# Optimization experiments

Measured on AMD Instinct MI355X. Metric: run time of the kernel, lower is better.

## Reference

```python
import jax, jax.numpy as jnp
import numpy as np

P = 16           # patch size
D = 768          # embed / feature dim (= 3*P*P)
T = 8            # number of task vectors
H_META = 192     # MetaNet hidden (= D // 4)


def patchify(x):
    # x: [B, 3, H, W] -> [B, N, 3*P*P]
    B, C, H, W = x.shape
    x = x.reshape(B, C, H // P, P, W // P, P)
    x = x.transpose(0, 2, 4, 1, 3, 5)
    return x.reshape(B, (H // P) * (W // P), C * P * P)


def encode(W1, b1, W2, b2, x):
    # base functional encoder f(params, x): shared weights over the batch
    patches = patchify(x)                       # [B, N, D]
    h = jax.nn.relu(patches @ W1 + b1)          # [B, N, D]
    pooled = h.mean(axis=1)                     # [B, D]
    return pooled @ W2 + b2                     # [B, D]


def setup_inputs() -> dict:
    key = jax.random.key(0)
    ks = jax.random.split(key, 14)
    B = 64
    s = 0.02
    return {
        "x":   jax.random.normal(ks[0], (B, 3, 224, 224), jnp.float32),
        # base model params
        "W1":  jax.random.normal(ks[1], (D, D), jnp.float32) * s,
        "b1":  jax.random.normal(ks[2], (D,), jnp.float32) * s,
        "W2":  jax.random.normal(ks[3], (D, D), jnp.float32) * s,
        "b2":  jax.random.normal(ks[4], (D,), jnp.float32) * s,
        # task-vector deltas (stacked over T tasks)
        "dW1": jax.random.normal(ks[5], (T, D, D), jnp.float32) * s,
        "db1": jax.random.normal(ks[6], (T, D), jnp.float32) * s,
        "dW2": jax.random.normal(ks[7], (T, D, D), jnp.float32) * s,
        "db2": jax.random.normal(ks[8], (T, D), jnp.float32) * s,
        # MetaNet (Linear-ReLU-Linear); zero-init in the original, random here
        "mw1": jax.random.normal(ks[9], (D, H_META), jnp.float32) * s,
        "mb1": jax.random.normal(ks[10], (H_META,), jnp.float32) * s,
        "mw2": jax.random.normal(ks[11], (H_META, T), jnp.float32) * s,
        "mb2": jax.random.normal(ks[12], (T,), jnp.float32) * s,
    }


def reference(x, W1, b1, W2, b2, dW1, db1, dW2, db2, mw1, mb1, mw2, mb2):
    # 1) base features with frozen base model (torch.no_grad)
    base = jax.lax.stop_gradient(encode(W1, b1, W2, b2, x))       # [B, D]
    # 2) per-sample mixing coefficients via MetaNet
    coefs = jax.nn.relu(base @ mw1 + mb1) @ mw2 + mb2             # [B, T]
    # 3) per-sample mixed parameters: p + sum_t c[b,t] * dp[t]
    nW1 = W1 + jnp.einsum("bt,tij->bij", coefs, dW1)              # [B, D, D]
    nb1 = b1 + coefs @ db1                                        # [B, D]
    nW2 = W2 + jnp.einsum("bt,tij->bij", coefs, dW2)              # [B, D, D]
    nb2 = b2 + coefs @ db2                                        # [B, D]
    # 4) batched per-sample forward with the mixed weights
    patches = patchify(x)                                         # [B, N, D]
    h = jax.nn.relu(jnp.einsum("bnd,bde->bne", patches, nW1) + nb1[:, None, :])
    pooled = h.mean(axis=1)                                       # [B, D]
    out = jnp.einsum("bd,bde->be", pooled, nW2) + nb2             # [B, D]
    return out
```

## Files before the change

kernel.cpp:

```cpp
#include <hip/hip_runtime.h>
#include <hip/hip_bf16.h>


typedef __bf16 bf16x8 __attribute__((ext_vector_type(8)));
typedef float f32x4 __attribute__((ext_vector_type(4)));
typedef __hip_bfloat16 bf16;

struct alignas(16) BF8 { bf16 h[8]; };

constexpr int BATCH = 64;
constexpr int NP    = 196;
constexpr int NPAD  = 256;
constexpr int DIM   = 768;
constexpr int NT    = 8;
constexpr size_t MSZ = (size_t)DIM * DIM;

__device__ __forceinline__ void async_cp16(const void* g, void* l) {
  __builtin_amdgcn_global_load_lds(
      (const __attribute__((address_space(1))) uint32_t*)g,
      (__attribute__((address_space(3))) uint32_t*)l, 16, 0, 0);
}

#define WAITVM(N) asm volatile("s_waitcnt vmcnt(" #N ")" ::: "memory")

constexpr int PREP_PATCH_BLOCKS = (BATCH * NPAD * (DIM / 4)) / 256;
constexpr int PREP_TRANS_BLOCKS = 24 * 24 * 18;

__global__ void k_prep(const float* __restrict__ x, bf16* __restrict__ A,
                       const float* __restrict__ W1, const float* __restrict__ dW1,
                       const float* __restrict__ W2, const float* __restrict__ dW2,
                       bf16* __restrict__ WT) {
  __shared__ float tile[32][33];
  int blk = blockIdx.x;
  int tid = threadIdx.x;
  if (blk < PREP_PATCH_BLOCKS) {
    int idx  = blk * 256 + tid;
    int col4 = idx % (DIM / 4);
    int row  = idx / (DIM / 4);
    int d = col4 * 4;
    int b = row >> 8;
    int n = row & 255;
    bf16 tmp[4];
    if (n < NP) {
      int hp = n / 14, wp = n % 14;
      int c  = d >> 8;
      int rr = d & 255;
      int i = rr >> 4, j = rr & 15;
      const float* src = x + ((((size_t)b * 3 + c) * 224 + hp * 16 + i) * 224 + wp * 16 + j);
      float4 f = *(const float4*)src;
      tmp[0] = __float2bfloat16(f.x);
      tmp[1] = __float2bfloat16(f.y);
      tmp[2] = __float2bfloat16(f.z);
      tmp[3] = __float2bfloat16(f.w);
    } else {
      tmp[0] = tmp[1] = tmp[2] = tmp[3] = __float2bfloat16(0.0f);
    }
    *(ushort4*)(A + (size_t)row * DIM + d) = *(ushort4*)tmp;
  } else {
    int tb  = blk - PREP_PATCH_BLOCKS;
    int mat = tb / 576;
    int rem = tb % 576;
    int n0 = (rem % 24) * 32;
    int k0 = (rem / 24) * 32;
    const float* src;
    if      (mat == 0) src = W1;
    else if (mat <= 8) src = dW1 + (size_t)(mat - 1) * MSZ;
    else if (mat == 9) src = W2;
    else               src = dW2 + (size_t)(mat - 10) * MSZ;
    int tx = tid & 31, ty = tid >> 5;
#pragma unroll
    for (int r = ty; r < 32; r += 8)
      tile[r][tx] = src[(size_t)(k0 + r) * DIM + n0 + tx];
    __syncthreads();
    bf16* dst = WT + (size_t)mat * MSZ;
#pragma unroll
    for (int r = ty; r < 32; r += 8)
      dst[(size_t)(n0 + r) * DIM + k0 + tx] = __float2bfloat16(tile[tx][r]);
  }
}

__global__ __launch_bounds__(512, 2)
void k_gemm_poolA(const bf16* __restrict__ A,
                  const bf16* __restrict__ WT,
                  const float* __restrict__ b1,
                  float* __restrict__ pooled) {
  __shared__ uint4 AslU[3][896];
  __shared__ uint4 BslU[3][768];
  __shared__ float red[8][48];

  int b  = blockIdx.x;
  int n0 = blockIdx.y * 192;
  int tid = threadIdx.x;
  int w = tid >> 6, lane = tid & 63;
  int quad = lane >> 4, l16 = lane & 15;
  int wm = w & 1, wn = w >> 1;

  const bf16* Ag = A + (size_t)b * NPAD * DIM;
  const bf16* Bg = WT + (size_t)n0 * DIM;

  f32x4 acc[7][3] = {};

  int off0, off1;
  {
    int s = w * 64 + lane;
    int p = s >> 3, u = (s & 7) ^ (p & 7);
    off0 = (2 * p + (u >> 2)) * DIM + (u & 3) * 8;
    int s1 = 512 + w * 64 + lane;
    int p1 = s1 >> 3, u1 = (s1 & 7) ^ (p1 & 7);
    off1 = (2 * p1 + (u1 >> 2)) * DIM + (u1 & 3) * 8;
  }
  auto stage_ab = [&](int buf, int kt) {
    const bf16* Ak = Ag + kt * 32;
    const bf16* Bk = Bg + kt * 32;
    async_cp16(Ak + off0, (void*)&AslU[buf][w * 64]);
    if (w < 6) async_cp16(Ak + off1, (void*)&AslU[buf][512 + w * 64]);
    async_cp16(Bk + off0, (void*)&BslU[buf][w * 64]);
    if (w < 4) async_cp16(Bk + off1, (void*)&BslU[buf][512 + w * 64]);
  };
  auto gslot = [&](int row, int kq) {
    return (size_t)((row >> 1) * 8 + ((4 * (row & 1) + kq) ^ ((row >> 1) & 7)));
  };

  stage_ab(0, 0);
  stage_ab(1, 1);
  WAITVM(0);
  __builtin_amdgcn_sched_barrier(0);

  int bufA = 0, stgA = 2;
  for (int kt = 0; kt < 24; kt++) {
    __builtin_amdgcn_s_barrier();
    if (kt < 22) stage_ab(stgA, kt + 2);
    __builtin_amdgcn_sched_barrier(0);
    const bf16* As = (const bf16*)AslU[bufA];
    const bf16* Bs = (const bf16*)BslU[bufA];
    bf16x8 bfr[3];
#pragma unroll
    for (int nf = 0; nf < 3; nf++) {
      int brow = wn * 48 + nf * 16 + l16;
      bfr[nf] = *(const bf16x8*)(Bs + gslot(brow, quad) * 8);
    }
    __builtin_amdgcn_s_setprio(1);
#pragma unroll
    for (int mf = 0; mf < 7; mf++) {
      int arow = wm * 112 + mf * 16 + l16;
      bf16x8 af = *(const bf16x8*)(As + gslot(arow, quad) * 8);
#pragma unroll
      for (int nf = 0; nf < 3; nf++)
        acc[mf][nf] = __builtin_amdgcn_mfma_f32_16x16x32_bf16(af, bfr[nf], acc[mf][nf], 0, 0, 0);
    }
    __builtin_amdgcn_s_setprio(0);
    if (kt < 22) {
      if (w < 4) WAITVM(4); else if (w < 6) WAITVM(3); else WAITVM(2);
    } else if (kt < 23) {
      WAITVM(0);
    }
    __builtin_amdgcn_sched_barrier(0);
    bufA = (bufA == 2) ? 0 : bufA + 1;
    stgA = (stgA == 2) ? 0 : stgA + 1;
  }

  float colsum[3];
#pragma unroll
  for (int nf = 0; nf < 3; nf++) {
    float bias = b1[n0 + wn * 48 + nf * 16 + l16];
    float s = 0.0f;
#pragma unroll
    for (int mf = 0; mf < 7; mf++) {
      int rbase = wm * 112 + mf * 16 + quad * 4;
#pragma unroll
      for (int r = 0; r < 4; r++) {
        if (rbase + r < NP) s += fmaxf(acc[mf][nf][r] + bias, 0.0f);
      }
    }
    s += __shfl_xor(s, 16, 64);
    s += __shfl_xor(s, 32, 64);
    colsum[nf] = s;
  }
  if (lane < 16) {
#pragma unroll
    for (int nf = 0; nf < 3; nf++) red[w][nf * 16 + lane] = colsum[nf];
  }
  __syncthreads();
  if (tid < 192) {
    int wn2 = tid / 48, off = tid % 48;
    float s = red[2 * wn2][off] + red[2 * wn2 + 1][off];
    pooled[(size_t)b * DIM + n0 + tid] = s * (1.0f / 196.0f);
  }
}

__global__ __launch_bounds__(256, 3)
void k_gemm_pool_mix(const bf16* __restrict__ A,
                     const bf16* __restrict__ WT,
                     const float* __restrict__ b1,
                     const float* __restrict__ db1,
                     const float* __restrict__ coefs,
                     float* __restrict__ pooled) {
  __shared__ uint4 AslU[3][896];
  __shared__ uint4 BslU[2][256];

  int b  = blockIdx.x;
  int n0 = blockIdx.y * 64;
  int tid = threadIdx.x;
  int wave = tid >> 6, lane = tid & 63;
  int quad = lane >> 4, l16 = lane & 15;

  float cr[NT];
#pragma unroll
  for (int t = 0; t < NT; t++) cr[t] = coefs[b * NT + t];

  const bf16* Ag = A + (size_t)b * NPAD * DIM;
  f32x4 acc[4][4] = {};

  int gbase = (wave < 2) ? wave * 256 : 512 + (wave - 2) * 192;
  int gcnt  = (wave < 2) ? 4 : 3;
  int aoff[4];
#pragma unroll
  for (int i = 0; i < 4; i++) {
    int s = gbase + i * 64 + lane;
    int p = s >> 3, u = (s & 7) ^ (p & 7);
    int r = 2 * p + (u >> 2), c = u & 3;
    aoff[i] = r * DIM + c * 8;
  }
  auto stage_a = [&](int buf, int kt) {
    const bf16* Ak = Ag + kt * 32;
#pragma unroll
    for (int i = 0; i < 4; i++) {
      if (i < gcnt)
        async_cp16(Ak + aoff[i], (void*)&AslU[buf][gbase + i * 64]);
    }
  };

  int bp = tid >> 3, bu = (tid & 7) ^ (bp & 7);
  int brow_st = 2 * bp + (bu >> 2), bcol_st = bu & 3;
  const bf16* Wrow = WT + (size_t)(n0 + brow_st) * DIM + bcol_st * 8;

  BF8 wreg[9];
  auto breg_load = [&](int kt) {
    const bf16* p0 = Wrow + kt * 32;
    wreg[0] = *(const BF8*)p0;
#pragma unroll
    for (int t = 0; t < NT; t++)
      wreg[1 + t] = *(const BF8*)(p0 + (size_t)(1 + t) * MSZ);
  };
  auto breg_write = [&](int buf) {
    float m[8];
#pragma unroll
    for (int j = 0; j < 8; j++) m[j] = __bfloat162float(wreg[0].h[j]);
#pragma unroll
    for (int t = 0; t < NT; t++) {
      float cc = cr[t];
#pragma unroll
      for (int j = 0; j < 8; j++) m[j] += cc * __bfloat162float(wreg[1 + t].h[j]);
    }
    BF8 o;
#pragma unroll
    for (int j = 0; j < 8; j++) o.h[j] = __float2bfloat16(m[j]);
    BslU[buf][tid] = *(uint4*)&o;
  };

  auto gslot = [&](int row, int kq) {
    return (size_t)((row >> 1) * 8 + ((4 * (row & 1) + kq) ^ ((row >> 1) & 7)));
  };

  stage_a(0, 0);
  stage_a(1, 1);
  breg_load(0);
  WAITVM(0);
  __builtin_amdgcn_sched_barrier(0);
  breg_write(0);
  asm volatile("s_waitcnt lgkmcnt(0)" ::: "memory");

  int bufA = 0, stgA = 2, bufB = 0;
  for (int kt = 0; kt < 24; kt++) {
    __builtin_amdgcn_s_barrier();
    if (kt < 23) breg_load(kt + 1);
    __builtin_amdgcn_sched_barrier(0);
    if (kt < 22) stage_a(stgA, kt + 2);
    __builtin_amdgcn_sched_barrier(0);
    const bf16* As = (const bf16*)AslU[bufA];
    const bf16* Bs = (const bf16*)BslU[bufB];
    bf16x8 bfr[4];
#pragma unroll
    for (int nf = 0; nf < 4; nf++) {
      int brow = nf * 16 + l16;
      bfr[nf] = *(const bf16x8*)(Bs + gslot(brow, quad) * 8);
    }
    __builtin_amdgcn_s_setprio(1);
#pragma unroll
    for (int mf = 0; mf < 4; mf++) {
      if (wave * 64 + mf * 16 < 224) {
        int arow = wave * 64 + mf * 16 + l16;
        bf16x8 af = *(const bf16x8*)(As + gslot(arow, quad) * 8);
#pragma unroll
        for (int nf = 0; nf < 4; nf++)
          acc[mf][nf] = __builtin_amdgcn_mfma_f32_16x16x32_bf16(af, bfr[nf], acc[mf][nf], 0, 0, 0);
      }
    }
    __builtin_amdgcn_s_setprio(0);
    if (kt < 22) {
      if (wave < 2) WAITVM(4); else WAITVM(3);
    } else if (kt < 23) {
      WAITVM(0);
    }
    __builtin_amdgcn_sched_barrier(0);
    if (kt < 23) {
      breg_write(bufB ^ 1);
      asm volatile("s_waitcnt lgkmcnt(0)" ::: "memory");
    }
    bufA = (bufA == 2) ? 0 : bufA + 1;
    stgA = (stgA == 2) ? 0 : stgA + 1;
    bufB ^= 1;
  }

  float* red = (float*)&BslU[0][0];
  int m0 = wave * 64;
  float colsum[4];
#pragma unroll
  for (int nf = 0; nf < 4; nf++) {
    int col = n0 + nf * 16 + l16;
    float bias = b1[col];
#pragma unroll
    for (int t = 0; t < NT; t++) bias += cr[t] * db1[t * DIM + col];
    float s = 0.0f;
#pragma unroll
    for (int mf = 0; mf < 4; mf++) {
      int rbase = m0 + mf * 16 + quad * 4;
#pragma unroll
      for (int r = 0; r < 4; r++) {
        if (rbase + r < NP) s += fmaxf(acc[mf][nf][r] + bias, 0.0f);
      }
    }
    s += __shfl_xor(s, 16, 64);
    s += __shfl_xor(s, 32, 64);
    colsum[nf] = s;
  }
  if (lane < 16) {
#pragma unroll
    for (int nf = 0; nf < 4; nf++) red[wave * 64 + nf * 16 + lane] = colsum[nf];
  }
  __syncthreads();
  if (tid < 64) {
    float s = red[tid] + red[64 + tid] + red[128 + tid] + red[192 + tid];
    pooled[(size_t)b * DIM + n0 + tid] = s * (1.0f / 196.0f);
  }
}

__global__ __launch_bounds__(256, 2)
void k_gemm2_ksplit(const float* __restrict__ Af,
                    const bf16* __restrict__ WT,
                    float* __restrict__ basep) {
  __shared__ uint4 AslU[64 * 8];
  __shared__ uint4 BslU[64 * 8];
  int n0  = blockIdx.x * 64;
  int kz  = blockIdx.y;
  int tid = threadIdx.x, wave = tid >> 6, lane = tid & 63;
  int quad = lane >> 4, l16 = lane & 15;
  f32x4 acc[4] = {};
  const bf16* Wm = WT + (size_t)9 * MSZ;
  for (int k0 = kz * 192; k0 < kz * 192 + 192; k0 += 64) {
#pragma unroll
    for (int i = 0; i < 2; i++) {
      int g = tid + i * 256;
      int r = g >> 3, c = g & 7;
      const float* src = Af + (size_t)r * DIM + k0 + c * 8;
      float4 xa = ((const float4*)src)[0];
      float4 xb = ((const float4*)src)[1];
      BF8 o;
      o.h[0] = __float2bfloat16(xa.x); o.h[1] = __float2bfloat16(xa.y);
      o.h[2] = __float2bfloat16(xa.z); o.h[3] = __float2bfloat16(xa.w);
      o.h[4] = __float2bfloat16(xb.x); o.h[5] = __float2bfloat16(xb.y);
      o.h[6] = __float2bfloat16(xb.z); o.h[7] = __float2bfloat16(xb.w);
      AslU[r * 8 + (c ^ (r & 7))] = *(uint4*)&o;
      BslU[r * 8 + (c ^ (r & 7))] = *(const uint4*)(Wm + (size_t)(n0 + r) * DIM + k0 + c * 8);
    }
    __syncthreads();
    const bf16* As = (const bf16*)AslU;
    const bf16* Bs = (const bf16*)BslU;
#pragma unroll
    for (int ks = 0; ks < 2; ks++) {
      int brow = wave * 16 + l16;
      bf16x8 bfr = *(const bf16x8*)(Bs + (size_t)(brow * 8 + ((ks * 4 + quad) ^ (brow & 7))) * 8);
#pragma unroll
      for (int mf = 0; mf < 4; mf++) {
        int arow = mf * 16 + l16;
        bf16x8 af = *(const bf16x8*)(As + (size_t)(arow * 8 + ((ks * 4 + quad) ^ (arow & 7))) * 8);
        acc[mf] = __builtin_amdgcn_mfma_f32_16x16x32_bf16(af, bfr, acc[mf], 0, 0, 0);
      }
    }
    __syncthreads();
  }
#pragma unroll
  for (int mf = 0; mf < 4; mf++) {
#pragma unroll
    for (int r = 0; r < 4; r++) {
      int row = mf * 16 + quad * 4 + r;
      int col = n0 + wave * 16 + l16;
      basep[((size_t)kz * 64 + row) * DIM + col] = acc[mf][r];
    }
  }
}

__global__ void k_metanet(const float* __restrict__ basep,
                          const float* __restrict__ b2,
                          const float* __restrict__ mw1, const float* __restrict__ mb1,
                          const float* __restrict__ mw2, const float* __restrict__ mb2,
                          float* __restrict__ coefs) {
  __shared__ float bl[DIM];
  __shared__ float hl[192];
  int b = blockIdx.x, tid = threadIdx.x;
  const size_t ZS = (size_t)64 * DIM;
  for (int i = tid; i < DIM; i += 192) {
    size_t o = (size_t)b * DIM + i;
    bl[i] = basep[o] + basep[ZS + o] + basep[2 * ZS + o] + basep[3 * ZS + o] + b2[i];
  }
  __syncthreads();
  float s = mb1[tid];
  for (int k = 0; k < DIM; k++) s += bl[k] * mw1[(size_t)k * 192 + tid];
  hl[tid] = fmaxf(s, 0.0f);
  __syncthreads();
  if (tid < NT) {
    float c = mb2[tid];
    for (int j = 0; j < 192; j++) c += hl[j] * mw2[(size_t)j * NT + tid];
    coefs[b * NT + tid] = c;
  }
}

__global__ __launch_bounds__(256, 2)
void k_gemm2(const float* __restrict__ Af,
             const bf16* __restrict__ WT,
             float* __restrict__ Y) {
  __shared__ uint4 AslU[64 * 8];
  __shared__ uint4 BslU[64 * 8];
  int n0  = blockIdx.x * 64;
  int mat = blockIdx.y;
  int tid = threadIdx.x, wave = tid >> 6, lane = tid & 63;
  int quad = lane >> 4, l16 = lane & 15;
  f32x4 acc[4] = {};
  const bf16* Wm = WT + (size_t)(9 + mat) * MSZ;
  for (int k0 = 0; k0 < DIM; k0 += 64) {
#pragma unroll
    for (int i = 0; i < 2; i++) {
      int g = tid + i * 256;
      int r = g >> 3, c = g & 7;
      const float* src = Af + (size_t)r * DIM + k0 + c * 8;
      float4 xa = ((const float4*)src)[0];
      float4 xb = ((const float4*)src)[1];
      BF8 o;
      o.h[0] = __float2bfloat16(xa.x); o.h[1] = __float2bfloat16(xa.y);
      o.h[2] = __float2bfloat16(xa.z); o.h[3] = __float2bfloat16(xa.w);
      o.h[4] = __float2bfloat16(xb.x); o.h[5] = __float2bfloat16(xb.y);
      o.h[6] = __float2bfloat16(xb.z); o.h[7] = __float2bfloat16(xb.w);
      AslU[r * 8 + (c ^ (r & 7))] = *(uint4*)&o;
      BslU[r * 8 + (c ^ (r & 7))] = *(const uint4*)(Wm + (size_t)(n0 + r) * DIM + k0 + c * 8);
    }
    __syncthreads();
    const bf16* As = (const bf16*)AslU;
    const bf16* Bs = (const bf16*)BslU;
#pragma unroll
    for (int ks = 0; ks < 2; ks++) {
      int brow = wave * 16 + l16;
      bf16x8 bfr = *(const bf16x8*)(Bs + (size_t)(brow * 8 + ((ks * 4 + quad) ^ (brow & 7))) * 8);
#pragma unroll
      for (int mf = 0; mf < 4; mf++) {
        int arow = mf * 16 + l16;
        bf16x8 af = *(const bf16x8*)(As + (size_t)(arow * 8 + ((ks * 4 + quad) ^ (arow & 7))) * 8);
        acc[mf] = __builtin_amdgcn_mfma_f32_16x16x32_bf16(af, bfr, acc[mf], 0, 0, 0);
      }
    }
    __syncthreads();
  }
#pragma unroll
  for (int mf = 0; mf < 4; mf++) {
#pragma unroll
    for (int r = 0; r < 4; r++) {
      int row = mf * 16 + quad * 4 + r;
      int col = n0 + wave * 16 + l16;
      Y[((size_t)mat * 64 + row) * DIM + col] = acc[mf][r];
    }
  }
}

__global__ void k_combine(const float* __restrict__ Y,
                          const float* __restrict__ coefs,
                          const float* __restrict__ b2,
                          const float* __restrict__ db2,
                          float* __restrict__ out) {
  int idx = blockIdx.x * 256 + threadIdx.x;
  int b = idx / DIM, e = idx % DIM;
  float v = Y[(size_t)b * DIM + e] + b2[e];
#pragma unroll
  for (int t = 0; t < NT; t++) {
    float c = coefs[b * NT + t];
    v += c * (Y[((size_t)(1 + t) * 64 + b) * DIM + e] + db2[(size_t)t * DIM + e]);
  }
  out[idx] = v;
}

extern "C" void kernel_launch(void* const* d_in, const int* in_sizes, int n_in,
                              void* d_out, int out_size, void* d_ws, size_t ws_size,
                              hipStream_t stream) {
  const float* x   = (const float*)d_in[0];
  const float* W1  = (const float*)d_in[1];
  const float* b1  = (const float*)d_in[2];
  const float* W2  = (const float*)d_in[3];
  const float* b2  = (const float*)d_in[4];
  const float* dW1 = (const float*)d_in[5];
  const float* db1 = (const float*)d_in[6];
  const float* dW2 = (const float*)d_in[7];
  const float* db2 = (const float*)d_in[8];
  const float* mw1 = (const float*)d_in[9];
  const float* mb1 = (const float*)d_in[10];
  const float* mw2 = (const float*)d_in[11];
  const float* mb2 = (const float*)d_in[12];
  float* out = (float*)d_out;
  (void)in_sizes; (void)n_in; (void)out_size; (void)ws_size;

  char* ws = (char*)d_ws;
  bf16*  A_bf    = (bf16*) (ws);
  bf16*  WT      = (bf16*) (ws + 25165824);
  float* pooledA = (float*)(ws + 46399488);
  float* pooledB = (float*)(ws + 46596096);
  float* coefs   = (float*)(ws + 46792704);
  float* basep   = (float*)(ws + 46794752);
  float* Y       = (float*)(ws + 47581184);

  k_prep<<<dim3(PREP_PATCH_BLOCKS + PREP_TRANS_BLOCKS), 256, 0, stream>>>(
      x, A_bf, W1, dW1, W2, dW2, WT);
  k_gemm_poolA<<<dim3(BATCH, DIM / 192), 512, 0, stream>>>(A_bf, WT, b1, pooledA);
  k_gemm2_ksplit<<<dim3(DIM / 64, 4), 256, 0, stream>>>(pooledA, WT, basep);
  k_metanet<<<dim3(BATCH), 192, 0, stream>>>(basep, b2, mw1, mb1, mw2, mb2, coefs);
  k_gemm_pool_mix<<<dim3(BATCH, DIM / 64), 256, 0, stream>>>(A_bf, WT, b1, db1, coefs, pooledB);
  k_gemm2<<<dim3(DIM / 64, 9), 256, 0, stream>>>(pooledB, WT, Y);
  k_combine<<<dim3((BATCH * DIM) / 256), 256, 0, stream>>>(Y, coefs, b2, db2, out);
}
```

Measured before the change: 286.4 us.

## Fold W2 into MetaNet first layer and deepen poolA pipeline to four stages

Precomputes G = W2·mw1 and the folded bias b2·mw1+mb1 inside the prep kernel, so the MetaNet hidden layer is computed directly from pooled features. This removes the split-K base GEMM launch and its partial-sum buffer. Separately, the first pooled GEMM moves from triple to quadruple buffering with adjusted vmcnt waits, while launch bounds drop to one block per SIMD occupancy target. The fold changes rounding (fp32 G instead of bf16 W2) and adds a serial 96-block fp32 GEMM to prep. The larger LDS footprint may also reduce occupancy.

```diff
diff --git a/kernel.cpp b/kernel.cpp
--- a/kernel.cpp
+++ b/kernel.cpp
@@ -25,12 +25,17 @@
 
 constexpr int PREP_PATCH_BLOCKS = (BATCH * NPAD * (DIM / 4)) / 256;
 constexpr int PREP_TRANS_BLOCKS = 24 * 24 * 18;
+constexpr int PREP_G_BLOCKS     = 96;
 
 __global__ void k_prep(const float* __restrict__ x, bf16* __restrict__ A,
                        const float* __restrict__ W1, const float* __restrict__ dW1,
                        const float* __restrict__ W2, const float* __restrict__ dW2,
-                       bf16* __restrict__ WT) {
+                       bf16* __restrict__ WT,
+                       const float* __restrict__ b2,
+                       const float* __restrict__ mw1, const float* __restrict__ mb1,
+                       float* __restrict__ Gbuf) {
   __shared__ float tile[32][33];
+  __shared__ float sG[8 * 768];
   int blk = blockIdx.x;
   int tid = threadIdx.x;
   if (blk < PREP_PATCH_BLOCKS) {
@@ -56,7 +61,7 @@
       tmp[0] = tmp[1] = tmp[2] = tmp[3] = __float2bfloat16(0.0f);
     }
     *(ushort4*)(A + (size_t)row * DIM + d) = *(ushort4*)tmp;
-  } else {
+  } else if (blk < PREP_PATCH_BLOCKS + PREP_TRANS_BLOCKS) {
     int tb  = blk - PREP_PATCH_BLOCKS;
     int mat = tb / 576;
     int rem = tb % 576;
@@ -76,16 +81,43 @@
 #pragma unroll
     for (int r = ty; r < 32; r += 8)
       dst[(size_t)(n0 + r) * DIM + k0 + tx] = __float2bfloat16(tile[tx][r]);
-  }
-}
-
-__global__ __launch_bounds__(512, 2)
+  } else {
+    int g = blk - (PREP_PATCH_BLOCKS + PREP_TRANS_BLOCKS);
+    int k0 = g * 8;
+    for (int i = tid; i < 8 * 768; i += 256)
+      sG[i] = W2[(size_t)(k0 + i / 768) * DIM + (i % 768)];
+    __syncthreads();
+    if (tid < 192) {
+      float accg[8] = {};
+      for (int n = 0; n < 768; n++) {
+        float m = mw1[(size_t)n * 192 + tid];
+#pragma unroll
+        for (int kk = 0; kk < 8; kk++) accg[kk] += sG[kk * 768 + n] * m;
+      }
+#pragma unroll
+      for (int kk = 0; kk < 8; kk++)
+        Gbuf[(size_t)(k0 + kk) * 192 + tid] = accg[kk];
+    }
+    if (g == 0) {
+      __syncthreads();
+      for (int i = tid; i < 768; i += 256) sG[i] = b2[i];
+      __syncthreads();
+      if (tid < 192) {
+        float s = mb1[tid];
+        for (int n = 0; n < 768; n++) s += sG[n] * mw1[(size_t)n * 192 + tid];
+        Gbuf[(size_t)768 * 192 + tid] = s;
+      }
+    }
+  }
+}
+
+__global__ __launch_bounds__(512, 1)
 void k_gemm_poolA(const bf16* __restrict__ A,
                   const bf16* __restrict__ WT,
                   const float* __restrict__ b1,
                   float* __restrict__ pooled) {
-  __shared__ uint4 AslU[3][896];
-  __shared__ uint4 BslU[3][768];
+  __shared__ uint4 AslU[4][896];
+  __shared__ uint4 BslU[4][768];
   __shared__ float red[8][48];
 
   int b  = blockIdx.x;
@@ -123,16 +155,17 @@
 
   stage_ab(0, 0);
   stage_ab(1, 1);
-  WAITVM(0);
+  stage_ab(2, 2);
+  if (w < 4) WAITVM(8); else if (w < 6) WAITVM(6); else WAITVM(4);
   __builtin_amdgcn_sched_barrier(0);
 
-  int bufA = 0, stgA = 2;
+  int cur = 0, stg = 3;
   for (int kt = 0; kt < 24; kt++) {
     __builtin_amdgcn_s_barrier();
-    if (kt < 22) stage_ab(stgA, kt + 2);
+    if (kt < 21) stage_ab(stg, kt + 3);
     __builtin_amdgcn_sched_barrier(0);
-    const bf16* As = (const bf16*)AslU[bufA];
-    const bf16* Bs = (const bf16*)BslU[bufA];
+    const bf16* As = (const bf16*)AslU[cur];
+    const bf16* Bs = (const bf16*)BslU[cur];
     bf16x8 bfr[3];
 #pragma unroll
     for (int nf = 0; nf < 3; nf++) {
@@ -149,14 +182,16 @@
         acc[mf][nf] = __builtin_amdgcn_mfma_f32_16x16x32_bf16(af, bfr[nf], acc[mf][nf], 0, 0, 0);
     }
     __builtin_amdgcn_s_setprio(0);
-    if (kt < 22) {
+    if (kt < 21) {
+      if (w < 4) WAITVM(8); else if (w < 6) WAITVM(6); else WAITVM(4);
+    } else if (kt == 21) {
       if (w < 4) WAITVM(4); else if (w < 6) WAITVM(3); else WAITVM(2);
-    } else if (kt < 23) {
+    } else if (kt == 22) {
       WAITVM(0);
     }
     __builtin_amdgcn_sched_barrier(0);
-    bufA = (bufA == 2) ? 0 : bufA + 1;
-    stgA = (stgA == 2) ? 0 : stgA + 1;
+    cur = (cur + 1) & 3;
+    stg = (stg + 1) & 3;
   }
 
   float colsum[3];
@@ -345,77 +380,17 @@
   }
 }
 
-__global__ __launch_bounds__(256, 2)
-void k_gemm2_ksplit(const float* __restrict__ Af,
-                    const bf16* __restrict__ WT,
-                    float* __restrict__ basep) {
-  __shared__ uint4 AslU[64 * 8];
-  __shared__ uint4 BslU[64 * 8];
-  int n0  = blockIdx.x * 64;
-  int kz  = blockIdx.y;
-  int tid = threadIdx.x, wave = tid >> 6, lane = tid & 63;
-  int quad = lane >> 4, l16 = lane & 15;
-  f32x4 acc[4] = {};
-  const bf16* Wm = WT + (size_t)9 * MSZ;
-  for (int k0 = kz * 192; k0 < kz * 192 + 192; k0 += 64) {
-#pragma unroll
-    for (int i = 0; i < 2; i++) {
-      int g = tid + i * 256;
-      int r = g >> 3, c = g & 7;
-      const float* src = Af + (size_t)r * DIM + k0 + c * 8;
-      float4 xa = ((const float4*)src)[0];
-      float4 xb = ((const float4*)src)[1];
-      BF8 o;
-      o.h[0] = __float2bfloat16(xa.x); o.h[1] = __float2bfloat16(xa.y);
-      o.h[2] = __float2bfloat16(xa.z); o.h[3] = __float2bfloat16(xa.w);
-      o.h[4] = __float2bfloat16(xb.x); o.h[5] = __float2bfloat16(xb.y);
-      o.h[6] = __float2bfloat16(xb.z); o.h[7] = __float2bfloat16(xb.w);
-      AslU[r * 8 + (c ^ (r & 7))] = *(uint4*)&o;
-      BslU[r * 8 + (c ^ (r & 7))] = *(const uint4*)(Wm + (size_t)(n0 + r) * DIM + k0 + c * 8);
-    }
-    __syncthreads();
-    const bf16* As = (const bf16*)AslU;
-    const bf16* Bs = (const bf16*)BslU;
-#pragma unroll
-    for (int ks = 0; ks < 2; ks++) {
-      int brow = wave * 16 + l16;
-      bf16x8 bfr = *(const bf16x8*)(Bs + (size_t)(brow * 8 + ((ks * 4 + quad) ^ (brow & 7))) * 8);
-#pragma unroll
-      for (int mf = 0; mf < 4; mf++) {
-        int arow = mf * 16 + l16;
-        bf16x8 af = *(const bf16x8*)(As + (size_t)(arow * 8 + ((ks * 4 + quad) ^ (arow & 7))) * 8);
-        acc[mf] = __builtin_amdgcn_mfma_f32_16x16x32_bf16(af, bfr, acc[mf], 0, 0, 0);
-      }
-    }
-    __syncthreads();
-  }
-#pragma unroll
-  for (int mf = 0; mf < 4; mf++) {
-#pragma unroll
-    for (int r = 0; r < 4; r++) {
-      int row = mf * 16 + quad * 4 + r;
-      int col = n0 + wave * 16 + l16;
-      basep[((size_t)kz * 64 + row) * DIM + col] = acc[mf][r];
-    }
-  }
-}
-
-__global__ void k_metanet(const float* __restrict__ basep,
-                          const float* __restrict__ b2,
-                          const float* __restrict__ mw1, const float* __restrict__ mb1,
+__global__ void k_metanet(const float* __restrict__ pooledA,
+                          const float* __restrict__ Gbuf,
                           const float* __restrict__ mw2, const float* __restrict__ mb2,
                           float* __restrict__ coefs) {
-  __shared__ float bl[DIM];
+  __shared__ float pl[DIM];
   __shared__ float hl[192];
   int b = blockIdx.x, tid = threadIdx.x;
-  const size_t ZS = (size_t)64 * DIM;
-  for (int i = tid; i < DIM; i += 192) {
-    size_t o = (size_t)b * DIM + i;
-    bl[i] = basep[o] + basep[ZS + o] + basep[2 * ZS + o] + basep[3 * ZS + o] + b2[i];
-  }
+  for (int i = tid; i < DIM; i += 192) pl[i] = pooledA[(size_t)b * DIM + i];
   __syncthreads();
-  float s = mb1[tid];
-  for (int k = 0; k < DIM; k++) s += bl[k] * mw1[(size_t)k * 192 + tid];
+  float s = Gbuf[(size_t)768 * 192 + tid];
+  for (int k = 0; k < DIM; k++) s += pl[k] * Gbuf[(size_t)k * 192 + tid];
   hl[tid] = fmaxf(s, 0.0f);
   __syncthreads();
   if (tid < NT) {
@@ -521,14 +496,13 @@
   float* pooledA = (float*)(ws + 46399488);
   float* pooledB = (float*)(ws + 46596096);
   float* coefs   = (float*)(ws + 46792704);
-  float* basep   = (float*)(ws + 46794752);
-  float* Y       = (float*)(ws + 47581184);
-
-  k_prep<<<dim3(PREP_PATCH_BLOCKS + PREP_TRANS_BLOCKS), 256, 0, stream>>>(
-      x, A_bf, W1, dW1, W2, dW2, WT);
+  float* Gbuf    = (float*)(ws + 46794752);
+  float* Y       = (float*)(ws + 47385344);
+
+  k_prep<<<dim3(PREP_PATCH_BLOCKS + PREP_TRANS_BLOCKS + PREP_G_BLOCKS), 256, 0, stream>>>(
+      x, A_bf, W1, dW1, W2, dW2, WT, b2, mw1, mb1, Gbuf);
   k_gemm_poolA<<<dim3(BATCH, DIM / 192), 512, 0, stream>>>(A_bf, WT, b1, pooledA);
-  k_gemm2_ksplit<<<dim3(DIM / 64, 4), 256, 0, stream>>>(pooledA, WT, basep);
-  k_metanet<<<dim3(BATCH), 192, 0, stream>>>(basep, b2, mw1, mb1, mw2, mb2, coefs);
+  k_metanet<<<dim3(BATCH), 192, 0, stream>>>(pooledA, Gbuf, mw2, mb2, coefs);
   k_gemm_pool_mix<<<dim3(BATCH, DIM / 64), 256, 0, stream>>>(A_bf, WT, b1, db1, coefs, pooledB);
   k_gemm2<<<dim3(DIM / 64, 9), 256, 0, stream>>>(pooledB, WT, Y);
   k_combine<<<dim3((BATCH * DIM) / 256), 256, 0, stream>>>(Y, coefs, b2, db2, out);
```

Result: slower. 357.5 us (+24.8%).
